# Kernel tuning notes

Hardware: AMD Instinct MI355X
Metric: run time of the kernel (lower is better)

The kernel has to match this reference:

```python
import jax, jax.numpy as jnp
import numpy as np

EPS = 1e-8  # torch.nn.CosineSimilarity default eps

def setup_inputs() -> dict:
    key = jax.random.key(0)
    k1, k2 = jax.random.split(key)
    B, R, T, D = 256, 36, 64, 1024
    img_feats = jax.random.normal(k1, (B, R, D), dtype=jnp.float32)
    cap_feats = jax.random.normal(k2, (B, T, D), dtype=jnp.float32)
    cap_mask = jnp.ones((B, T), dtype=jnp.float32)  # unused by the original forward
    return {"img_feats": img_feats, "cap_feats": cap_feats, "cap_mask": cap_mask}

def reference(img_feats, cap_feats, cap_mask):
    # img_feats: (B, R, D); cap_feats: (B, T, D)
    # cosine similarity between every region r and every caption word t:
    # scores[b, r, t] = (img[b,r] . cap[b,t]) / max(||img[b,r]|| * ||cap[b,t]||, eps)
    dots = jnp.einsum('brd,btd->brt', img_feats, cap_feats)
    img_norm = jnp.linalg.norm(img_feats, axis=-1)  # (B, R)
    cap_norm = jnp.linalg.norm(cap_feats, axis=-1)  # (B, T)
    denom = jnp.maximum(img_norm[:, :, None] * cap_norm[:, None, :], EPS)
    scores = dots / denom  # (B, R, T)
    # softmax over regions (dim=1 in the original)
    attn = jax.nn.softmax(scores, axis=1)  # (B, R, T)
    # weighted sum over regions -> per-word image representation (B, T, D)
    img_cap_reps = jnp.einsum('brt,brd->btd', attn, img_feats)
    return img_cap_reps
```

## Files before the change

### kernel.cpp

```cpp
#include <hip/hip_runtime.h>

#define RREG 36
#define TTOK 64
#define DDIM 1024

typedef __attribute__((ext_vector_type(4))) float f32x4;
typedef __attribute__((ext_vector_type(8))) short bf16x8;

__device__ __forceinline__ unsigned short f2bf(float x) {
  unsigned int u = __float_as_uint(x);
  u += 0x7fffu + ((u >> 16) & 1u);
  return (unsigned short)(u >> 16);
}

__global__ __launch_bounds__(1024) void scan_fused(
    const float* __restrict__ img, const float* __restrict__ cap,
    float* __restrict__ out) {
  __shared__ __align__(16) unsigned char smem[52032];

  unsigned short* scap  = (unsigned short*)(smem + 0);
  unsigned short* simg  = (unsigned short*)(smem + 17408);
  unsigned short* simgT = (unsigned short*)(smem + 0);
  float* ssc            = (float*)(smem + 32768);
  unsigned short* satt  = (unsigned short*)(smem + 45440);
  float* sni            = (float*)(smem + 51584);
  float* snc            = (float*)(smem + 51776);

  const int tid  = threadIdx.x;
  const int lane = tid & 63;
  const int wave = tid >> 6;
  const int fm   = lane & 15;
  const int kq   = lane >> 4;
  const int b    = blockIdx.x;

  const float* imgb = img + (size_t)b * RREG * DDIM;
  const float* capb = cap + (size_t)b * TTOK * DDIM;
  float*       outb = out + (size_t)b * TTOK * DDIM;

  const int mt = wave >> 2;
  const int nt = wave & 3;

  f32x4 acc = {0.f, 0.f, 0.f, 0.f};
  float cn0 = 0.f, cn1 = 0.f, in0 = 0.f, in1 = 0.f;

  const int trow = tid >> 5;
  const int d4   = tid & 31;

  for (int c = 0; c < 8; ++c) {
    const int dbase = c * 128 + d4 * 4;
    {
      float4 v = *(const float4*)(capb + trow * DDIM + dbase);
      cn0 += v.x * v.x + v.y * v.y + v.z * v.z + v.w * v.w;
      ushort4 p; p.x = f2bf(v.x); p.y = f2bf(v.y); p.z = f2bf(v.z); p.w = f2bf(v.w);
      *(ushort4*)(scap + trow * 136 + d4 * 4) = p;

      float4 w = *(const float4*)(capb + (trow + 32) * DDIM + dbase);
      cn1 += w.x * w.x + w.y * w.y + w.z * w.z + w.w * w.w;
      ushort4 q; q.x = f2bf(w.x); q.y = f2bf(w.y); q.z = f2bf(w.z); q.w = f2bf(w.w);
      *(ushort4*)(scap + (trow + 32) * 136 + d4 * 4) = q;
    }
    {
      float4 v = *(const float4*)(imgb + trow * DDIM + dbase);
      in0 += v.x * v.x + v.y * v.y + v.z * v.z + v.w * v.w;
      ushort4 p; p.x = f2bf(v.x); p.y = f2bf(v.y); p.z = f2bf(v.z); p.w = f2bf(v.w);
      *(ushort4*)(simg + trow * 136 + d4 * 4) = p;
      if (tid < 512) {
        int r2 = trow + 32;
        float4 w = make_float4(0.f, 0.f, 0.f, 0.f);
        if (r2 < RREG) {
          w = *(const float4*)(imgb + r2 * DDIM + dbase);
          in1 += w.x * w.x + w.y * w.y + w.z * w.z + w.w * w.w;
        }
        ushort4 q; q.x = f2bf(w.x); q.y = f2bf(w.y); q.z = f2bf(w.z); q.w = f2bf(w.w);
        *(ushort4*)(simg + r2 * 136 + d4 * 4) = q;
      }
    }
    __syncthreads();
    if (wave < 12) {
      const unsigned short* arow = simg + (mt * 16 + fm) * 136 + kq * 8;
      const unsigned short* brow = scap + (nt * 16 + fm) * 136 + kq * 8;
#pragma unroll
      for (int ks = 0; ks < 4; ++ks) {
        bf16x8 av = *(const bf16x8*)(arow + ks * 32);
        bf16x8 bv = *(const bf16x8*)(brow + ks * 32);
        acc = __builtin_amdgcn_mfma_f32_16x16x32_bf16(av, bv, acc, 0, 0, 0);
      }
    }
    __syncthreads();
  }

  if (wave < 12) {
#pragma unroll
    for (int i = 0; i < 4; ++i)
      ssc[(mt * 16 + kq * 4 + i) * 66 + nt * 16 + fm] = acc[i];
  }
#pragma unroll
  for (int off = 16; off > 0; off >>= 1) {
    cn0 += __shfl_down(cn0, off, 32);
    cn1 += __shfl_down(cn1, off, 32);
    in0 += __shfl_down(in0, off, 32);
    in1 += __shfl_down(in1, off, 32);
  }
  if ((tid & 31) == 0) {
    snc[trow]      = sqrtf(cn0);
    snc[trow + 32] = sqrtf(cn1);
    sni[trow]      = sqrtf(in0);
    if (trow < 16) sni[trow + 32] = sqrtf(in1);
  }
  __syncthreads();

  if (wave == 0) {
    float cn = snc[lane];
    float s[RREG];
    float mx = -1e30f;
#pragma unroll
    for (int r = 0; r < RREG; ++r) {
      float denom = fmaxf(sni[r] * cn, 1e-8f);
      float v = ssc[r * 66 + lane] / denom;
      s[r] = v;
      mx = fmaxf(mx, v);
    }
    float sum = 0.f;
#pragma unroll
    for (int r = 0; r < RREG; ++r) { float e = __expf(s[r] - mx); s[r] = e; sum += e; }
    float rinv = 1.f / sum;
    unsigned short* ap = satt + lane * 48;
#pragma unroll
    for (int r = 0; r < RREG; ++r) ap[r] = f2bf(s[r] * rinv);
#pragma unroll
    for (int r = RREG; r < 48; ++r) ap[r] = 0;
  }
  __syncthreads();

  const int mtB = wave >> 2;
  const unsigned short* arowB = satt + (mtB * 16 + fm) * 48;
  bf16x8 a1 = *(const bf16x8*)(arowB + kq * 8);
  bf16x8 a2 = {0, 0, 0, 0, 0, 0, 0, 0};
  if (kq < 2) a2 = *(const bf16x8*)(arowB + 32 + kq * 8);

  for (int cb = 0; cb < 8; ++cb) {
    __syncthreads();
    for (int f = tid; f < 1536; f += 1024) {
      int g = f & 511;
      int r = (f >> 9) * 16 + (g & 15);
      int qd = (g >> 4) & 3;
      int sd = g >> 6;
      int dloc = (qd + 4 * sd) * 4;
      float4 v = make_float4(0.f, 0.f, 0.f, 0.f);
      if (r < RREG) v = *(const float4*)(imgb + r * DDIM + cb * 128 + dloc);
      simgT[(dloc + 0) * 56 + r] = f2bf(v.x);
      simgT[(dloc + 1) * 56 + r] = f2bf(v.y);
      simgT[(dloc + 2) * 56 + r] = f2bf(v.z);
      simgT[(dloc + 3) * 56 + r] = f2bf(v.w);
    }
    __syncthreads();
#pragma unroll
    for (int j = 0; j < 2; ++j) {
      int ntB = (wave & 3) * 2 + j;
      const unsigned short* brow = simgT + (ntB * 16 + fm) * 56;
      bf16x8 b1 = *(const bf16x8*)(brow + kq * 8);
      bf16x8 b2 = {0, 0, 0, 0, 0, 0, 0, 0};
      if (kq < 2) b2 = *(const bf16x8*)(brow + 32 + kq * 8);
      f32x4 o = {0.f, 0.f, 0.f, 0.f};
      o = __builtin_amdgcn_mfma_f32_16x16x32_bf16(a1, b1, o, 0, 0, 0);
      o = __builtin_amdgcn_mfma_f32_16x16x32_bf16(a2, b2, o, 0, 0, 0);
#pragma unroll
      for (int i = 0; i < 4; ++i)
        outb[(mtB * 16 + kq * 4 + i) * DDIM + cb * 128 + ntB * 16 + fm] = o[i];
    }
  }
}

extern "C" void kernel_launch(void* const* d_in, const int* in_sizes, int n_in,
                              void* d_out, int out_size, void* d_ws, size_t ws_size,
                              hipStream_t stream) {
  const float* img = (const float*)d_in[0];
  const float* cap = (const float*)d_in[1];
  float* out = (float*)d_out;
  scan_fused<<<dim3(256), dim3(1024), 0, stream>>>(img, cap, out);
}
```

Before: 162.5 us.

## Split fused kernel into attention and output kernels with more blocks

Replaces the single 256-block, 1024-thread fused kernel with two kernels. The first computes dot products and norms straight from registers into MFMA (no LDS staging) and writes bf16 softmax weights to workspace. The second reads those weights and the image features to produce the output, using 1024 blocks per kernel to raise occupancy and parallelism. In exchange, image features are re-read once per caption-token quarter, there is an extra launch plus a workspace round trip, and the second kernel does strided scalar global loads of img.

```diff
diff --git a/kernel.cpp b/kernel.cpp
--- a/kernel.cpp
+++ b/kernel.cpp
@@ -1,11 +1,34 @@
 #include <hip/hip_runtime.h>
+#include <hip/hip_bf16.h>
 
+#define DDIM 1024
 #define RREG 36
 #define TTOK 64
-#define DDIM 1024
+#define KPAD 48
 
 typedef __attribute__((ext_vector_type(4))) float f32x4;
 typedef __attribute__((ext_vector_type(8))) short bf16x8;
+
+__device__ __forceinline__ float sq4(float4 v) {
+  return v.x * v.x + v.y * v.y + v.z * v.z + v.w * v.w;
+}
+
+__device__ __forceinline__ bf16x8 cvt8(float4 a, float4 b) {
+  union { bf16x8 v; __hip_bfloat162 h[4]; } u;
+  u.h[0] = __float22bfloat162_rn(make_float2(a.x, a.y));
+  u.h[1] = __float22bfloat162_rn(make_float2(a.z, a.w));
+  u.h[2] = __float22bfloat162_rn(make_float2(b.x, b.y));
+  u.h[3] = __float22bfloat162_rn(make_float2(b.z, b.w));
+  return u.v;
+}
+
+__device__ __forceinline__ bf16x8 pack8(const float* v) {
+  union { bf16x8 x; __hip_bfloat162 h[4]; } u;
+#pragma unroll
+  for (int i = 0; i < 4; ++i)
+    u.h[i] = __float22bfloat162_rn(make_float2(v[2 * i], v[2 * i + 1]));
+  return u.x;
+}
 
 __device__ __forceinline__ unsigned short f2bf(float x) {
   unsigned int u = __float_as_uint(x);
@@ -13,161 +36,144 @@
   return (unsigned short)(u >> 16);
 }
 
-__global__ __launch_bounds__(1024) void scan_fused(
+__global__ __launch_bounds__(192) void scan_attn(
     const float* __restrict__ img, const float* __restrict__ cap,
-    float* __restrict__ out) {
-  __shared__ __align__(16) unsigned char smem[52032];
-
-  unsigned short* scap  = (unsigned short*)(smem + 0);
-  unsigned short* simg  = (unsigned short*)(smem + 17408);
-  unsigned short* simgT = (unsigned short*)(smem + 0);
-  float* ssc            = (float*)(smem + 32768);
-  unsigned short* satt  = (unsigned short*)(smem + 45440);
-  float* sni            = (float*)(smem + 51584);
-  float* snc            = (float*)(smem + 51776);
+    unsigned short* __restrict__ attnw) {
+  __shared__ float sdots[16][52];
+  __shared__ float sni[KPAD];
+  __shared__ float snc[16];
 
   const int tid  = threadIdx.x;
   const int lane = tid & 63;
   const int wave = tid >> 6;
   const int fm   = lane & 15;
   const int kq   = lane >> 4;
-  const int b    = blockIdx.x;
+  const int b    = blockIdx.x >> 2;
+  const int t0   = (blockIdx.x & 3) << 4;
 
+  const float* capb = cap + (size_t)b * TTOK * DDIM;
   const float* imgb = img + (size_t)b * RREG * DDIM;
-  const float* capb = cap + (size_t)b * TTOK * DDIM;
-  float*       outb = out + (size_t)b * TTOK * DDIM;
 
-  const int mt = wave >> 2;
-  const int nt = wave & 3;
+  const int t = t0 + fm;
+  const int r = wave * 16 + fm;
+  const bool rv = (r < RREG);
 
-  f32x4 acc = {0.f, 0.f, 0.f, 0.f};
-  float cn0 = 0.f, cn1 = 0.f, in0 = 0.f, in1 = 0.f;
+  const float* aptr = capb + t * DDIM + kq * 8;
+  const float* bptr = imgb + (rv ? r : 0) * DDIM + kq * 8;
 
-  const int trow = tid >> 5;
-  const int d4   = tid & 31;
+  f32x4 acc0 = {0.f, 0.f, 0.f, 0.f}, acc1 = {0.f, 0.f, 0.f, 0.f};
+  float cn = 0.f, inrm = 0.f;
 
-  for (int c = 0; c < 8; ++c) {
-    const int dbase = c * 128 + d4 * 4;
-    {
-      float4 v = *(const float4*)(capb + trow * DDIM + dbase);
-      cn0 += v.x * v.x + v.y * v.y + v.z * v.z + v.w * v.w;
-      ushort4 p; p.x = f2bf(v.x); p.y = f2bf(v.y); p.z = f2bf(v.z); p.w = f2bf(v.w);
-      *(ushort4*)(scap + trow * 136 + d4 * 4) = p;
+#pragma unroll 2
+  for (int kc = 0; kc < 16; ++kc) {
+    float4 a0 = *(const float4*)(aptr);
+    float4 a1 = *(const float4*)(aptr + 4);
+    float4 a2 = *(const float4*)(aptr + 32);
+    float4 a3 = *(const float4*)(aptr + 36);
+    float4 b0 = make_float4(0.f, 0.f, 0.f, 0.f), b1 = b0, b2 = b0, b3 = b0;
+    if (rv) {
+      b0 = *(const float4*)(bptr);
+      b1 = *(const float4*)(bptr + 4);
+      b2 = *(const float4*)(bptr + 32);
+      b3 = *(const float4*)(bptr + 36);
+    }
+    aptr += 64; bptr += 64;
+    cn   += sq4(a0) + sq4(a1) + sq4(a2) + sq4(a3);
+    inrm += sq4(b0) + sq4(b1) + sq4(b2) + sq4(b3);
+    acc0 = __builtin_amdgcn_mfma_f32_16x16x32_bf16(cvt8(a0, a1), cvt8(b0, b1), acc0, 0, 0, 0);
+    acc1 = __builtin_amdgcn_mfma_f32_16x16x32_bf16(cvt8(a2, a3), cvt8(b2, b3), acc1, 0, 0, 0);
+  }
+  acc0 += acc1;
 
-      float4 w = *(const float4*)(capb + (trow + 32) * DDIM + dbase);
-      cn1 += w.x * w.x + w.y * w.y + w.z * w.z + w.w * w.w;
-      ushort4 q; q.x = f2bf(w.x); q.y = f2bf(w.y); q.z = f2bf(w.z); q.w = f2bf(w.w);
-      *(ushort4*)(scap + (trow + 32) * 136 + d4 * 4) = q;
-    }
-    {
-      float4 v = *(const float4*)(imgb + trow * DDIM + dbase);
-      in0 += v.x * v.x + v.y * v.y + v.z * v.z + v.w * v.w;
-      ushort4 p; p.x = f2bf(v.x); p.y = f2bf(v.y); p.z = f2bf(v.z); p.w = f2bf(v.w);
-      *(ushort4*)(simg + trow * 136 + d4 * 4) = p;
-      if (tid < 512) {
-        int r2 = trow + 32;
-        float4 w = make_float4(0.f, 0.f, 0.f, 0.f);
-        if (r2 < RREG) {
-          w = *(const float4*)(imgb + r2 * DDIM + dbase);
-          in1 += w.x * w.x + w.y * w.y + w.z * w.z + w.w * w.w;
-        }
-        ushort4 q; q.x = f2bf(w.x); q.y = f2bf(w.y); q.z = f2bf(w.z); q.w = f2bf(w.w);
-        *(ushort4*)(simg + r2 * 136 + d4 * 4) = q;
-      }
-    }
-    __syncthreads();
-    if (wave < 12) {
-      const unsigned short* arow = simg + (mt * 16 + fm) * 136 + kq * 8;
-      const unsigned short* brow = scap + (nt * 16 + fm) * 136 + kq * 8;
-#pragma unroll
-      for (int ks = 0; ks < 4; ++ks) {
-        bf16x8 av = *(const bf16x8*)(arow + ks * 32);
-        bf16x8 bv = *(const bf16x8*)(brow + ks * 32);
-        acc = __builtin_amdgcn_mfma_f32_16x16x32_bf16(av, bv, acc, 0, 0, 0);
-      }
-    }
-    __syncthreads();
-  }
-
-  if (wave < 12) {
-#pragma unroll
-    for (int i = 0; i < 4; ++i)
-      ssc[(mt * 16 + kq * 4 + i) * 66 + nt * 16 + fm] = acc[i];
+  cn   += __shfl_xor(cn, 16);   cn   += __shfl_xor(cn, 32);
+  inrm += __shfl_xor(inrm, 16); inrm += __shfl_xor(inrm, 32);
+  if (lane < 16) {
+    sni[wave * 16 + fm] = sqrtf(inrm);
+    if (wave == 0) snc[fm] = sqrtf(cn);
   }
 #pragma unroll
-  for (int off = 16; off > 0; off >>= 1) {
-    cn0 += __shfl_down(cn0, off, 32);
-    cn1 += __shfl_down(cn1, off, 32);
-    in0 += __shfl_down(in0, off, 32);
-    in1 += __shfl_down(in1, off, 32);
-  }
-  if ((tid & 31) == 0) {
-    snc[trow]      = sqrtf(cn0);
-    snc[trow + 32] = sqrtf(cn1);
-    sni[trow]      = sqrtf(in0);
-    if (trow < 16) sni[trow + 32] = sqrtf(in1);
-  }
+  for (int i = 0; i < 4; ++i)
+    sdots[kq * 4 + i][wave * 16 + fm] = acc0[i];
   __syncthreads();
 
-  if (wave == 0) {
-    float cn = snc[lane];
-    float s[RREG];
+  if (tid < 16) {
+    const float cnv = snc[tid];
+    float sc[RREG];
     float mx = -1e30f;
 #pragma unroll
-    for (int r = 0; r < RREG; ++r) {
-      float denom = fmaxf(sni[r] * cn, 1e-8f);
-      float v = ssc[r * 66 + lane] / denom;
-      s[r] = v;
+    for (int rr = 0; rr < RREG; ++rr) {
+      float dnm = fmaxf(sni[rr] * cnv, 1e-8f);
+      float v = sdots[tid][rr] / dnm;
+      sc[rr] = v;
       mx = fmaxf(mx, v);
     }
     float sum = 0.f;
 #pragma unroll
-    for (int r = 0; r < RREG; ++r) { float e = __expf(s[r] - mx); s[r] = e; sum += e; }
-    float rinv = 1.f / sum;
-    unsigned short* ap = satt + lane * 48;
+    for (int rr = 0; rr < RREG; ++rr) {
+      float ev = __expf(sc[rr] - mx);
+      sc[rr] = ev;
+      sum += ev;
+    }
+    const float rinv = 1.f / sum;
+    unsigned short* arow = attnw + ((size_t)b * TTOK + t0 + tid) * KPAD;
 #pragma unroll
-    for (int r = 0; r < RREG; ++r) ap[r] = f2bf(s[r] * rinv);
+    for (int r0 = 0; r0 < RREG; r0 += 4) {
+      ushort4 p;
+      p.x = f2bf(sc[r0 + 0] * rinv);
+      p.y = f2bf(sc[r0 + 1] * rinv);
+      p.z = f2bf(sc[r0 + 2] * rinv);
+      p.w = f2bf(sc[r0 + 3] * rinv);
+      *(ushort4*)(arow + r0) = p;
+    }
+    ushort4 zz; zz.x = 0; zz.y = 0; zz.z = 0; zz.w = 0;
+    *(ushort4*)(arow + 36) = zz;
+    *(ushort4*)(arow + 40) = zz;
+    *(ushort4*)(arow + 44) = zz;
+  }
+}
+
+__global__ __launch_bounds__(256) void scan_out(
+    const float* __restrict__ img, const unsigned short* __restrict__ attnw,
+    float* __restrict__ out) {
+  const int tid  = threadIdx.x;
+  const int lane = tid & 63;
+  const int wave = tid >> 6;
+  const int fm   = lane & 15;
+  const int kq   = lane >> 4;
+  const int b    = blockIdx.x >> 2;
+  const int d0   = (blockIdx.x & 3) << 8;
+
+  const float* imgb = img + (size_t)b * RREG * DDIM;
+  const unsigned short* attb = attnw + (size_t)b * TTOK * KPAD;
+  float* outb = out + (size_t)b * TTOK * DDIM;
+
+  const unsigned short* ap = attb + (wave * 16 + fm) * KPAD;
+  bf16x8 zf = {0, 0, 0, 0, 0, 0, 0, 0};
+  bf16x8 af0 = *(const bf16x8*)(ap + kq * 8);
+  bf16x8 af1 = zf;
+  if (kq < 2) af1 = *(const bf16x8*)(ap + 32 + kq * 8);
+
+  for (int s = 0; s < 16; ++s) {
+    const int d = d0 + s * 16 + fm;
+    float v[8];
 #pragma unroll
-    for (int r = RREG; r < 48; ++r) ap[r] = 0;
-  }
-  __syncthreads();
-
-  const int mtB = wave >> 2;
-  const unsigned short* arowB = satt + (mtB * 16 + fm) * 48;
-  bf16x8 a1 = *(const bf16x8*)(arowB + kq * 8);
-  bf16x8 a2 = {0, 0, 0, 0, 0, 0, 0, 0};
-  if (kq < 2) a2 = *(const bf16x8*)(arowB + 32 + kq * 8);
-
-  for (int cb = 0; cb < 8; ++cb) {
-    __syncthreads();
-    for (int f = tid; f < 1536; f += 1024) {
-      int g = f & 511;
-      int r = (f >> 9) * 16 + (g & 15);
-      int qd = (g >> 4) & 3;
-      int sd = g >> 6;
-      int dloc = (qd + 4 * sd) * 4;
-      float4 v = make_float4(0.f, 0.f, 0.f, 0.f);
-      if (r < RREG) v = *(const float4*)(imgb + r * DDIM + cb * 128 + dloc);
-      simgT[(dloc + 0) * 56 + r] = f2bf(v.x);
-      simgT[(dloc + 1) * 56 + r] = f2bf(v.y);
-      simgT[(dloc + 2) * 56 + r] = f2bf(v.z);
-      simgT[(dloc + 3) * 56 + r] = f2bf(v.w);
+    for (int j = 0; j < 8; ++j) v[j] = imgb[(kq * 8 + j) * DDIM + d];
+    bf16x8 bf0 = pack8(v);
+    bf16x8 bf1 = zf;
+    if (kq == 0) {
+      float w[8];
+#pragma unroll
+      for (int j = 0; j < 4; ++j) w[j] = imgb[(32 + j) * DDIM + d];
+#pragma unroll
+      for (int j = 4; j < 8; ++j) w[j] = 0.f;
+      bf1 = pack8(w);
     }
-    __syncthreads();
+    f32x4 o = {0.f, 0.f, 0.f, 0.f};
+    o = __builtin_amdgcn_mfma_f32_16x16x32_bf16(af0, bf0, o, 0, 0, 0);
+    o = __builtin_amdgcn_mfma_f32_16x16x32_bf16(af1, bf1, o, 0, 0, 0);
+    float* op = outb + (wave * 16 + kq * 4) * DDIM + d;
 #pragma unroll
-    for (int j = 0; j < 2; ++j) {
-      int ntB = (wave & 3) * 2 + j;
-      const unsigned short* brow = simgT + (ntB * 16 + fm) * 56;
-      bf16x8 b1 = *(const bf16x8*)(brow + kq * 8);
-      bf16x8 b2 = {0, 0, 0, 0, 0, 0, 0, 0};
-      if (kq < 2) b2 = *(const bf16x8*)(brow + 32 + kq * 8);
-      f32x4 o = {0.f, 0.f, 0.f, 0.f};
-      o = __builtin_amdgcn_mfma_f32_16x16x32_bf16(a1, b1, o, 0, 0, 0);
-      o = __builtin_amdgcn_mfma_f32_16x16x32_bf16(a2, b2, o, 0, 0, 0);
-#pragma unroll
-      for (int i = 0; i < 4; ++i)
-        outb[(mtB * 16 + kq * 4 + i) * DDIM + cb * 128 + ntB * 16 + fm] = o[i];
-    }
+    for (int i = 0; i < 4; ++i) op[i * DDIM] = o[i];
   }
 }
 
@@ -177,5 +183,8 @@
   const float* img = (const float*)d_in[0];
   const float* cap = (const float*)d_in[1];
   float* out = (float*)d_out;
-  scan_fused<<<dim3(256), dim3(1024), 0, stream>>>(img, cap, out);
+  unsigned short* attnw = (unsigned short*)d_ws;
+
+  scan_attn<<<dim3(1024), dim3(192), 0, stream>>>(img, cap, attnw);
+  scan_out<<<dim3(1024), dim3(256), 0, stream>>>(img, attnw, out);
 }
```

New measurement: 178.9 us. 1.1x slower.
